# Optimization experiments

Hardware: AMD Instinct MI355X
Metric: run time of the kernel (lower is better)

The kernel has to match this reference:

```python
import jax, jax.numpy as jnp
import numpy as np

WS, SHIFT, NH, DIM = 8, 4, 4, 128
HD = DIM // NH
B, H, W = 16, 128, 128
N = WS * WS
LOG100 = float(np.log(100.0))


def _rel_tables():
    r = np.arange(-(WS - 1), WS, dtype=np.float32)
    tab = np.stack(np.meshgrid(r, r, indexing='ij'), axis=-1) / (WS - 1) * 8.0
    tab = np.sign(tab) * np.log2(np.abs(tab) + 1.0) / np.log2(8.0)
    coords = np.stack(np.meshgrid(np.arange(WS), np.arange(WS), indexing='ij')).reshape(2, -1)
    rel = (coords[:, :, None] - coords[:, None, :]).transpose(1, 2, 0).copy()
    rel[:, :, 0] += WS - 1
    rel[:, :, 1] += WS - 1
    rel[:, :, 0] *= 2 * WS - 1
    return jnp.asarray(tab.reshape(-1, 2)), jnp.asarray(rel.sum(-1))

REL_TABLE, REL_INDEX = _rel_tables()  # ((2WS-1)^2, 2), (N, N)


def _attn_mask():
    img = np.zeros((H, W), np.float32)
    cnt = 0
    for hs in (slice(0, -WS), slice(-WS, -SHIFT), slice(-SHIFT, None)):
        for ws in (slice(0, -WS), slice(-WS, -SHIFT), slice(-SHIFT, None)):
            img[hs, ws] = cnt
            cnt += 1
    mw = img.reshape(H // WS, WS, W // WS, WS).transpose(0, 2, 1, 3).reshape(-1, N)
    d = mw[:, None, :] - mw[:, :, None]
    return jnp.asarray(np.where(d != 0, -100.0, 0.0).astype(np.float32))

ATTN_MASK = _attn_mask()  # (nW, N, N)


def _ln(x, w, b, eps=1e-5):
    mu = x.mean(-1, keepdims=True)
    var = ((x - mu) ** 2).mean(-1, keepdims=True)
    return (x - mu) * jax.lax.rsqrt(var + eps) * w + b


def setup_inputs() -> dict:
    key = jax.random.key(0)
    ks = jax.random.split(key, 8)
    s = 0.02
    return {
        'x': jax.random.normal(ks[0], (B, DIM, H, W), jnp.float32),
        'norm1_w': jnp.ones((DIM,), jnp.float32),
        'norm1_b': jnp.zeros((DIM,), jnp.float32),
        'qkv_w': jax.random.normal(ks[1], (3 * DIM, DIM), jnp.float32) * s,
        'q_bias': jnp.zeros((DIM,), jnp.float32),
        'v_bias': jnp.zeros((DIM,), jnp.float32),
        'logit_scale': jnp.full((NH, 1, 1), float(np.log(10.0)), jnp.float32),
        'cpb_w1': jax.random.normal(ks[2], (512, 2), jnp.float32) * s,
        'cpb_b1': jnp.zeros((512,), jnp.float32),
        'cpb_w2': jax.random.normal(ks[3], (NH, 512), jnp.float32) * s,
        'proj_w': jax.random.normal(ks[4], (DIM, DIM), jnp.float32) * s,
        'proj_b': jnp.zeros((DIM,), jnp.float32),
        'norm2_w': jnp.ones((DIM,), jnp.float32),
        'norm2_b': jnp.zeros((DIM,), jnp.float32),
        'fc1_w': jax.random.normal(ks[5], (4 * DIM, DIM), jnp.float32) * s,
        'fc1_b': jnp.zeros((4 * DIM,), jnp.float32),
        'fc2_w': jax.random.normal(ks[6], (DIM, 4 * DIM), jnp.float32) * s,
        'fc2_b': jnp.zeros((DIM,), jnp.float32),
    }


def reference(x, norm1_w, norm1_b, qkv_w, q_bias, v_bias, logit_scale,
              cpb_w1, cpb_b1, cpb_w2, proj_w, proj_b,
              norm2_w, norm2_b, fc1_w, fc1_b, fc2_w, fc2_b):
    xb = jnp.transpose(x, (0, 2, 3, 1))                 # (B,H,W,C)
    shortcut = xb.reshape(B, H * W, DIM)
    shifted = jnp.roll(xb, (-SHIFT, -SHIFT), axis=(1, 2))
    # window partition -> (B*nW, N, C)
    xw = shifted.reshape(B, H // WS, WS, W // WS, WS, DIM)
    xw = xw.transpose(0, 1, 3, 2, 4, 5).reshape(-1, N, DIM)
    B_ = xw.shape[0]
    qkv_bias = jnp.concatenate([q_bias, jnp.zeros_like(v_bias), v_bias])
    qkv = xw @ qkv_w.T + qkv_bias
    qkv = qkv.reshape(B_, N, 3, NH, HD).transpose(2, 0, 3, 1, 4)
    q, k, v = qkv[0], qkv[1], qkv[2]                    # (B_,NH,N,HD)
    qn = q / jnp.maximum(jnp.linalg.norm(q, axis=-1, keepdims=True), 1e-12)
    kn = k / jnp.maximum(jnp.linalg.norm(k, axis=-1, keepdims=True), 1e-12)
    attn = jnp.einsum('bhnd,bhmd->bhnm', qn, kn)
    attn = attn * jnp.exp(jnp.minimum(logit_scale, LOG100))
    # continuous relative position bias: tiny MLP over log-spaced coords + gather
    tab = jax.nn.relu(REL_TABLE @ cpb_w1.T + cpb_b1) @ cpb_w2.T    # ((2WS-1)^2, NH)
    bias = tab[REL_INDEX.reshape(-1)].reshape(N, N, NH).transpose(2, 0, 1)
    attn = attn + (16.0 * jax.nn.sigmoid(bias))[None]
    nW = ATTN_MASK.shape[0]
    attn = attn.reshape(B_ // nW, nW, NH, N, N) + ATTN_MASK[None, :, None]
    attn = jax.nn.softmax(attn.reshape(B_, NH, N, N), axis=-1)
    out = jnp.einsum('bhnm,bhmd->bhnd', attn, v).transpose(0, 2, 1, 3).reshape(B_, N, DIM)
    out = out @ proj_w.T + proj_b
    # window reverse + reverse cyclic shift
    out = out.reshape(B, H // WS, W // WS, WS, WS, DIM).transpose(0, 1, 3, 2, 4, 5).reshape(B, H, W, DIM)
    out = jnp.roll(out, (SHIFT, SHIFT), axis=(1, 2)).reshape(B, H * W, DIM)
    x1 = shortcut + _ln(out, norm1_w, norm1_b)          # Swin-v2 post-norm residual
    hdn = jax.nn.silu(x1 @ fc1_w.T + fc1_b) @ fc2_w.T + fc2_b
    x2 = x1 + _ln(hdn, norm2_w, norm2_b)
    return x2.reshape(B, H, W, DIM).transpose(0, 3, 1, 2)
```

## Files before the change

kernel.cpp:

```cpp
#include <hip/hip_runtime.h>
#include <cstdint>
#include <cstddef>

typedef __bf16 bf16;
typedef __bf16 bf16x4 __attribute__((ext_vector_type(4)));
typedef __bf16 bf16x8 __attribute__((ext_vector_type(8)));
typedef float f32x4 __attribute__((ext_vector_type(4)));

#define MFMA16(a, b, c) __builtin_amdgcn_mfma_f32_16x16x32_bf16((a), (b), (c), 0, 0, 0)

__device__ __forceinline__ float bf2f(bf16 v) { return (float)v; }

__device__ __forceinline__ void pack4(float a0, float a1, float a2, float a3, bf16* dst) {
    bf16x4 v; v[0] = (bf16)a0; v[1] = (bf16)a1; v[2] = (bf16)a2; v[3] = (bf16)a3;
    *(bf16x4*)dst = v;
}

#define OFF_SCALES 65536
#define OFF_FLAG   65552
#define OFF_QKVB   65600
#define OFF_PROJB  67136
#define OFF_N1W    67648
#define OFF_N1B    68160
#define OFF_FC1B   68672
#define OFF_FC2B   70720
#define OFF_N2W    71232
#define OFF_N2B    71744
#define OFF_QKVW   73728
#define OFF_PROJW  172032
#define OFF_FC1W   204800
#define OFF_FC2W   335872

template<int DT>
__device__ __forceinline__ void g_ld4(const void* base, size_t idx, float* o) {
    if constexpr (DT == 0) {
        uint2 d = *(const uint2*)((const bf16*)base + idx);
        const bf16* p = (const bf16*)&d;
        o[0] = bf2f(p[0]); o[1] = bf2f(p[1]); o[2] = bf2f(p[2]); o[3] = bf2f(p[3]);
    } else {
        float4 d = *(const float4*)((const float*)base + idx);
        o[0] = d.x; o[1] = d.y; o[2] = d.z; o[3] = d.w;
    }
}

__global__ void k_init(const void* __restrict__ cpb_w1, const void* __restrict__ cpb_b1,
                       const void* __restrict__ cpb_w2, const void* __restrict__ logit_scale,
                       const void* __restrict__ qkv_w, const void* __restrict__ proj_w,
                       const void* __restrict__ fc1w, const void* __restrict__ fc2w,
                       const void* __restrict__ q_bias, const void* __restrict__ v_bias,
                       const void* __restrict__ proj_b, const void* __restrict__ n1w, const void* __restrict__ n1b,
                       const void* __restrict__ fc1b, const void* __restrict__ fc2b,
                       const void* __restrict__ n2w, const void* __restrict__ n2b,
                       char* __restrict__ ws)
{
    const int t = threadIdx.x;
    __shared__ int s_cnt;
    if (t == 0) s_cnt = 0;
    __syncthreads();
    {
        const unsigned short* u = (const unsigned short*)qkv_w;
        int c = 0;
        for (int i = t; i < 1024; i += 256) {
            const int e = (u[i] >> 7) & 0xFF;
            if (e >= 0x90 || (e != 0 && e <= 0x60)) ++c;
        }
        atomicAdd(&s_cnt, c);
    }
    __syncthreads();
    const int isf = (s_cnt > 64) ? 1 : 0;

    if (blockIdx.x == 0) {
        float* biasAll = (float*)ws;
        float* scales  = (float*)(ws + OFF_SCALES);
        int*   flag    = (int*)(ws + OFF_FLAG);
        if (t == 0) *flag = isf;
        __shared__ float w1s[1024];
        __shared__ float b1s[512];
        __shared__ float w2s[2048];
        __shared__ float tabv[225][4];
        if (isf) {
            const float* w1 = (const float*)cpb_w1;
            const float* b1 = (const float*)cpb_b1;
            const float* w2 = (const float*)cpb_w2;
            for (int i = t; i < 1024; i += 256) w1s[i] = w1[i];
            for (int i = t; i < 512;  i += 256) b1s[i] = b1[i];
            for (int i = t; i < 2048; i += 256) w2s[i] = w2[i];
            if (t < 4) scales[t] = expf(fminf(((const float*)logit_scale)[t], 4.6051701859880914f));
        } else {
            const bf16* w1 = (const bf16*)cpb_w1;
            const bf16* b1 = (const bf16*)cpb_b1;
            const bf16* w2 = (const bf16*)cpb_w2;
            for (int i = t; i < 1024; i += 256) w1s[i] = bf2f(w1[i]);
            for (int i = t; i < 512;  i += 256) b1s[i] = bf2f(b1[i]);
            for (int i = t; i < 2048; i += 256) w2s[i] = bf2f(w2[i]);
            if (t < 4) scales[t] = expf(fminf(bf2f(((const bf16*)logit_scale)[t]), 4.6051701859880914f));
        }
        __syncthreads();
        if (t < 225) {
            const int i = t / 15, j = t % 15;
            auto relf = [](int tt) -> float {
                float tf = (float)tt * (8.0f / 7.0f);
                float a = log2f(fabsf(tf) + 1.0f) * (1.0f / 3.0f);
                return tt < 0 ? -a : a;
            };
            const float x0 = relf(i - 7), x1 = relf(j - 7);
            float a0 = 0.f, a1 = 0.f, a2 = 0.f, a3 = 0.f;
            for (int jj = 0; jj < 512; ++jj) {
                float hv = w1s[jj*2] * x0 + w1s[jj*2+1] * x1 + b1s[jj];
                hv = fmaxf(hv, 0.0f);
                a0 += w2s[jj]        * hv;
                a1 += w2s[512 + jj]  * hv;
                a2 += w2s[1024 + jj] * hv;
                a3 += w2s[1536 + jj] * hv;
            }
            tabv[t][0] = a0; tabv[t][1] = a1; tabv[t][2] = a2; tabv[t][3] = a3;
        }
        __syncthreads();
        for (int idx = t; idx < 4*64*64; idx += 256) {
            const int h = idx >> 12, rem = idx & 4095, i = rem >> 6, j = rem & 63;
            const int di = (i >> 3) - (j >> 3) + 7;
            const int dj = (i & 7) - (j & 7) + 7;
            const float bv = tabv[di*15 + dj][h];
            biasAll[idx] = 16.0f / (1.0f + expf(-bv));
        }
    } else {
        const int g  = (blockIdx.x - 1) * 256 + t;
        const int gs = 96 * 256;
        bf16* qw = (bf16*)(ws + OFF_QKVW);
        bf16* pw = (bf16*)(ws + OFF_PROJW);
        bf16* f1 = (bf16*)(ws + OFF_FC1W);
        bf16* f2 = (bf16*)(ws + OFF_FC2W);
        if (isf) {
            const float* a = (const float*)qkv_w;  for (int i = g; i < 49152; i += gs) qw[i] = (bf16)a[i];
            const float* b = (const float*)proj_w; for (int i = g; i < 16384; i += gs) pw[i] = (bf16)b[i];
            const float* c = (const float*)fc1w;   for (int i = g; i < 65536; i += gs) f1[i] = (bf16)c[i];
            const float* d = (const float*)fc2w;   for (int i = g; i < 65536; i += gs) f2[i] = (bf16)d[i];
        } else {
            const bf16* a = (const bf16*)qkv_w;  for (int i = g; i < 49152; i += gs) qw[i] = a[i];
            const bf16* b = (const bf16*)proj_w; for (int i = g; i < 16384; i += gs) pw[i] = b[i];
            const bf16* c = (const bf16*)fc1w;   for (int i = g; i < 65536; i += gs) f1[i] = c[i];
            const bf16* d = (const bf16*)fc2w;   for (int i = g; i < 65536; i += gs) f2[i] = d[i];
        }
        auto ldf = [&](const void* p, int i) -> float {
            return isf ? ((const float*)p)[i] : bf2f(((const bf16*)p)[i]);
        };
        float* qb  = (float*)(ws + OFF_QKVB);
        float* pb  = (float*)(ws + OFF_PROJB);
        float* w1  = (float*)(ws + OFF_N1W);
        float* b1  = (float*)(ws + OFF_N1B);
        float* f1b = (float*)(ws + OFF_FC1B);
        float* f2b = (float*)(ws + OFF_FC2B);
        float* w2  = (float*)(ws + OFF_N2W);
        float* b2  = (float*)(ws + OFF_N2B);
        for (int i = g; i < 384; i += gs)
            qb[i] = (i < 128) ? ldf(q_bias, i) : ((i < 256) ? 0.0f : ldf(v_bias, i - 256));
        for (int i = g; i < 512; i += gs) f1b[i] = ldf(fc1b, i);
        for (int i = g; i < 128; i += gs) {
            pb[i]  = ldf(proj_b, i); w1[i] = ldf(n1w, i); b1[i] = ldf(n1b, i);
            f2b[i] = ldf(fc2b, i);   w2[i] = ldf(n2w, i); b2[i] = ldf(n2b, i);
        }
    }
}

__global__ __launch_bounds__(256, 2) void k_fused(
    const void* __restrict__ x,
    const bf16* __restrict__ qkvw, const float* __restrict__ qkvb,
    const bf16* __restrict__ projw, const float* __restrict__ projb,
    const float* __restrict__ n1wf, const float* __restrict__ n1bf,
    const bf16* __restrict__ fc1w, const float* __restrict__ fc1bf,
    const bf16* __restrict__ fc2w, const float* __restrict__ fc2bf,
    const float* __restrict__ n2wf, const float* __restrict__ n2bf,
    const float* __restrict__ biasAll, const float* __restrict__ scales,
    const int* __restrict__ flag, void* __restrict__ out)
{
    const int isf = *flag;

    __shared__ __align__(16) char smem[75008];
    bf16* Xs    = (bf16*)smem;
    bf16* qkvs  = (bf16*)(smem + 17408);
    bf16* PsT   = qkvs;
    bf16* x1s   = qkvs;
    bf16* vs    = (bf16*)(smem + 54272);
    bf16* Os    = vs;
    bf16* hs    = vs;
    float* invqs = (float*)(smem + 72704);
    float* invks = (float*)(smem + 73728);
    int*   rid   = (int*)(smem + 74752);
    float* psum = invqs;
    float* pvar = invks;

    const int tid  = threadIdx.x;
    const int wv   = tid >> 6;
    const int lane = tid & 63;
    const int l15  = lane & 15;
    const int quad = lane >> 4;

    const int bid0 = blockIdx.x;
    const int bid  = ((bid0 & 7) << 9) | (bid0 >> 3);
    const int b   = bid >> 8;
    const int wh  = (bid >> 4) & 15;
    const int ww  = bid & 15;

    {
        const int c  = tid & 127;
        const int rb = tid >> 7;
        const int w0 = ww*8 + 4;
        const int w1 = (ww*8 + 8) & 127;
#pragma unroll
        for (int k = 0; k < 4; ++k) {
            const int r    = k*2 + rb;
            const int srch = (wh*8 + r + 4) & 127;
            const size_t rowbase = (((size_t)(b*128 + c))*128 + srch)*128;
            float va[4], vb[4];
            if (isf) { g_ld4<1>(x, rowbase + w0, va); g_ld4<1>(x, rowbase + w1, vb); }
            else     { g_ld4<0>(x, rowbase + w0, va); g_ld4<0>(x, rowbase + w1, vb); }
#pragma unroll
            for (int j = 0; j < 4; ++j) {
                Xs[(r*8 + j)*136 + c]     = (bf16)va[j];
                Xs[(r*8 + 4 + j)*136 + c] = (bf16)vb[j];
            }
        }
        if (tid < 64) {
            const int rr = tid >> 3, cc = tid & 7;
            const int hs_ = wh*8 + rr, wsc = ww*8 + cc;
            const int rh = (hs_ < 120) ? 0 : ((hs_ < 124) ? 1 : 2);
            const int rw = (wsc < 120) ? 0 : ((wsc < 124) ? 1 : 2);
            rid[tid] = rh*3 + rw;
        }
    }
    __syncthreads();

    {
        f32x4 acc[6][4];
#pragma unroll
        for (int nl = 0; nl < 6; ++nl)
#pragma unroll
            for (int mt = 0; mt < 4; ++mt) acc[nl][mt] = (f32x4){0.f, 0.f, 0.f, 0.f};
#pragma unroll
        for (int ks = 0; ks < 4; ++ks) {
            bf16x8 a[4];
#pragma unroll
            for (int mt = 0; mt < 4; ++mt)
                a[mt] = *(const bf16x8*)&Xs[(mt*16 + l15)*136 + ks*32 + quad*8];
#pragma unroll
            for (int nl = 0; nl < 6; ++nl) {
                const int tile = wv*6 + nl;
                bf16x8 bw = *(const bf16x8*)&qkvw[(size_t)(tile*16 + l15)*128 + ks*32 + quad*8];
                if (tile < 16) {
#pragma unroll
                    for (int mt = 0; mt < 4; ++mt)
                        acc[nl][mt] = MFMA16(bw, a[mt], acc[nl][mt]);
                } else {
#pragma unroll
                    for (int mt = 0; mt < 4; ++mt)
                        acc[nl][mt] = MFMA16(a[mt], bw, acc[nl][mt]);
                }
            }
        }
#pragma unroll
        for (int nl = 0; nl < 6; ++nl) {
            const int tile = wv*6 + nl;
            const int ctb  = tile*16;
            if (ctb < 256) {
                const float4 qb4 = *(const float4*)&qkvb[ctb + quad*4];
#pragma unroll
                for (int mt = 0; mt < 4; ++mt)
                    pack4(acc[nl][mt][0] + qb4.x, acc[nl][mt][1] + qb4.y,
                          acc[nl][mt][2] + qb4.z, acc[nl][mt][3] + qb4.w,
                          &qkvs[(mt*16 + l15)*264 + ctb + quad*4]);
            } else {
                const float bb = qkvb[ctb + l15];
#pragma unroll
                for (int mt = 0; mt < 4; ++mt)
                    pack4(acc[nl][mt][0] + bb, acc[nl][mt][1] + bb,
                          acc[nl][mt][2] + bb, acc[nl][mt][3] + bb,
                          &vs[(ctb - 256 + l15)*72 + mt*16 + quad*4]);
            }
        }
    }
    __syncthreads();

    {
        const int n = lane;
        const bf16* qrow = &qkvs[n*264 + wv*32];
        const bf16* krow = &qkvs[n*264 + 128 + wv*32];
        float sq = 0.f, sk = 0.f;
#pragma unroll
        for (int dd = 0; dd < 4; ++dd) {
            bf16x8 vq = *(const bf16x8*)(qrow + dd*8);
            bf16x8 vk = *(const bf16x8*)(krow + dd*8);
#pragma unroll
            for (int e = 0; e < 8; ++e) {
                const float fq = (float)vq[e]; sq += fq*fq;
                const float fk = (float)vk[e]; sk += fk*fk;
            }
        }
        invqs[wv*64 + n] = 1.0f / fmaxf(sqrtf(sq), 1e-12f);
        invks[wv*64 + n] = 1.0f / fmaxf(sqrtf(sk), 1e-12f);
    }
    __syncthreads();

    {
        const float scale = scales[wv];
        f32x4 s[4][4];
#pragma unroll
        for (int jt = 0; jt < 4; ++jt)
#pragma unroll
            for (int it = 0; it < 4; ++it) s[jt][it] = (f32x4){0.f, 0.f, 0.f, 0.f};
        bf16x8 aq[4];
#pragma unroll
        for (int it = 0; it < 4; ++it)
            aq[it] = *(const bf16x8*)&qkvs[(it*16 + l15)*264 + wv*32 + quad*8];
#pragma unroll
        for (int jt = 0; jt < 4; ++jt) {
            bf16x8 bk = *(const bf16x8*)&qkvs[(jt*16 + l15)*264 + 128 + wv*32 + quad*8];
#pragma unroll
            for (int it = 0; it < 4; ++it)
                s[jt][it] = MFMA16(bk, aq[it], s[jt][it]);
        }
        __syncthreads();

        const float* bg = biasAll + wv*4096;
        const bool bnd = (wh == 15) || (ww == 15);
        float iqs[4]; int ri[4];
#pragma unroll
        for (int it = 0; it < 4; ++it) {
            iqs[it] = invqs[wv*64 + it*16 + l15] * scale;
            ri[it]  = rid[it*16 + l15];
        }
        float4 ikj[4]; int4 rj4[4];
#pragma unroll
        for (int jt = 0; jt < 4; ++jt) {
            ikj[jt] = *(const float4*)&invks[wv*64 + jt*16 + quad*4];
            rj4[jt] = *(const int4*)&rid[jt*16 + quad*4];
        }
#pragma unroll
        for (int it = 0; it < 4; ++it) {
            const int i = it*16 + l15;
#pragma unroll
            for (int jt = 0; jt < 4; ++jt) {
                const float4 bb = *(const float4*)&bg[i*64 + jt*16 + quad*4];
#pragma unroll
                for (int r = 0; r < 4; ++r) {
                    float v = s[jt][it][r] * (iqs[it] * ((const float*)&ikj[jt])[r]) + ((const float*)&bb)[r];
                    if (bnd && (ri[it] != ((const int*)&rj4[jt])[r])) v -= 100.0f;
                    s[jt][it][r] = v;
                }
            }
            float m = s[0][it][0];
#pragma unroll
            for (int jt = 0; jt < 4; ++jt)
#pragma unroll
                for (int r = 0; r < 4; ++r) m = fmaxf(m, s[jt][it][r]);
            m = fmaxf(m, __shfl_xor(m, 16));
            m = fmaxf(m, __shfl_xor(m, 32));
            float sm = 0.f;
#pragma unroll
            for (int jt = 0; jt < 4; ++jt)
#pragma unroll
                for (int r = 0; r < 4; ++r) {
                    const float e = __expf(s[jt][it][r] - m);
                    s[jt][it][r] = e;
                    sm += e;
                }
            sm += __shfl_xor(sm, 16);
            sm += __shfl_xor(sm, 32);
            const float inv = 1.0f / sm;
#pragma unroll
            for (int jt = 0; jt < 4; ++jt)
                pack4(s[jt][it][0]*inv, s[jt][it][1]*inv, s[jt][it][2]*inv, s[jt][it][3]*inv,
                      &PsT[wv*4608 + i*72 + jt*16 + quad*4]);
        }
    }
    __syncthreads();

    {
        f32x4 o[2][4];
#pragma unroll
        for (int dt = 0; dt < 2; ++dt)
#pragma unroll
            for (int it = 0; it < 4; ++it) o[dt][it] = (f32x4){0.f, 0.f, 0.f, 0.f};
#pragma unroll
        for (int ks = 0; ks < 2; ++ks) {
            bf16x8 bp[4];
#pragma unroll
            for (int it = 0; it < 4; ++it)
                bp[it] = *(const bf16x8*)&PsT[wv*4608 + (it*16 + l15)*72 + ks*32 + quad*8];
#pragma unroll
            for (int dt = 0; dt < 2; ++dt) {
                bf16x8 av = *(const bf16x8*)&vs[(wv*32 + dt*16 + l15)*72 + ks*32 + quad*8];
#pragma unroll
                for (int it = 0; it < 4; ++it)
                    o[dt][it] = MFMA16(av, bp[it], o[dt][it]);
            }
        }
        __syncthreads();
#pragma unroll
        for (int dt = 0; dt < 2; ++dt)
#pragma unroll
            for (int it = 0; it < 4; ++it)
                pack4(o[dt][it][0], o[dt][it][1], o[dt][it][2], o[dt][it][3],
                      &Os[(it*16 + l15)*136 + wv*32 + dt*16 + quad*4]);
    }
    __syncthreads();

    {
        f32x4 pa[2][4];
#pragma unroll
        for (int ct = 0; ct < 2; ++ct)
#pragma unroll
            for (int tt = 0; tt < 4; ++tt) pa[ct][tt] = (f32x4){0.f, 0.f, 0.f, 0.f};
#pragma unroll
        for (int ks = 0; ks < 4; ++ks) {
            bf16x8 bo[4];
#pragma unroll
            for (int tt = 0; tt < 4; ++tt)
                bo[tt] = *(const bf16x8*)&Os[(tt*16 + l15)*136 + ks*32 + quad*8];
#pragma unroll
            for (int ct = 0; ct < 2; ++ct) {
                bf16x8 aw = *(const bf16x8*)&projw[(size_t)(wv*32 + ct*16 + l15)*128 + ks*32 + quad*8];
#pragma unroll
                for (int tt = 0; tt < 4; ++tt)
                    pa[ct][tt] = MFMA16(aw, bo[tt], pa[ct][tt]);
            }
        }
        float4 pb4[2], wn4[2], bn4[2];
#pragma unroll
        for (int ct = 0; ct < 2; ++ct) {
            const int ob = wv*32 + ct*16 + quad*4;
            pb4[ct] = *(const float4*)&projb[ob];
            wn4[ct] = *(const float4*)&n1wf[ob];
            bn4[ct] = *(const float4*)&n1bf[ob];
        }
#pragma unroll
        for (int tt = 0; tt < 4; ++tt) {
            float sv = 0.f;
#pragma unroll
            for (int ct = 0; ct < 2; ++ct)
#pragma unroll
                for (int r = 0; r < 4; ++r) {
                    pa[ct][tt][r] += ((const float*)&pb4[ct])[r];
                    sv += pa[ct][tt][r];
                }
            sv += __shfl_xor(sv, 16);
            sv += __shfl_xor(sv, 32);
            if (quad == 0) psum[wv*64 + tt*16 + l15] = sv;
        }
        __syncthreads();
        float mu[4];
#pragma unroll
        for (int tt = 0; tt < 4; ++tt) {
            const int tok = tt*16 + l15;
            mu[tt] = (psum[tok] + psum[64+tok] + psum[128+tok] + psum[192+tok]) * (1.0f/128.0f);
            float sv = 0.f;
#pragma unroll
            for (int ct = 0; ct < 2; ++ct)
#pragma unroll
                for (int r = 0; r < 4; ++r) {
                    const float d = pa[ct][tt][r] - mu[tt];
                    sv += d*d;
                }
            sv += __shfl_xor(sv, 16);
            sv += __shfl_xor(sv, 32);
            if (quad == 0) pvar[wv*64 + tok] = sv;
        }
        __syncthreads();
#pragma unroll
        for (int tt = 0; tt < 4; ++tt) {
            const int tok = tt*16 + l15;
            const float var = (pvar[tok] + pvar[64+tok] + pvar[128+tok] + pvar[192+tok]) * (1.0f/128.0f);
            const float rstd = rsqrtf(var + 1e-5f);
#pragma unroll
            for (int ct = 0; ct < 2; ++ct) {
                const int ob = wv*32 + ct*16 + quad*4;
                bf16x4 xr = *(const bf16x4*)&Xs[tok*136 + ob];
                float xv[4];
#pragma unroll
                for (int r = 0; r < 4; ++r)
                    xv[r] = bf2f(xr[r]) + (pa[ct][tt][r] - mu[tt]) * rstd * ((const float*)&wn4[ct])[r]
                            + ((const float*)&bn4[ct])[r];
                pack4(xv[0], xv[1], xv[2], xv[3], &x1s[tok*136 + ob]);
            }
        }
    }
    __syncthreads();

    f32x4 ya[2][4];
#pragma unroll
    for (int ct = 0; ct < 2; ++ct)
#pragma unroll
        for (int tt = 0; tt < 4; ++tt) ya[ct][tt] = (f32x4){0.f, 0.f, 0.f, 0.f};

#pragma unroll
    for (int ch = 0; ch < 4; ++ch) {
        if (ch) __syncthreads();
        f32x4 ha[2][4];
#pragma unroll
        for (int ht = 0; ht < 2; ++ht)
#pragma unroll
            for (int tt = 0; tt < 4; ++tt) ha[ht][tt] = (f32x4){0.f, 0.f, 0.f, 0.f};
#pragma unroll
        for (int ks = 0; ks < 4; ++ks) {
            bf16x8 bx[4];
#pragma unroll
            for (int tt = 0; tt < 4; ++tt)
                bx[tt] = *(const bf16x8*)&x1s[(tt*16 + l15)*136 + ks*32 + quad*8];
#pragma unroll
            for (int ht = 0; ht < 2; ++ht) {
                bf16x8 aw = *(const bf16x8*)&fc1w[(size_t)(ch*128 + wv*32 + ht*16 + l15)*128 + ks*32 + quad*8];
#pragma unroll
                for (int tt = 0; tt < 4; ++tt)
                    ha[ht][tt] = MFMA16(aw, bx[tt], ha[ht][tt]);
            }
        }
#pragma unroll
        for (int ht = 0; ht < 2; ++ht) {
            const float4 bb4 = *(const float4*)&fc1bf[ch*128 + wv*32 + ht*16 + quad*4];
            const int hb = wv*32 + ht*16 + quad*4;
#pragma unroll
            for (int tt = 0; tt < 4; ++tt) {
                float hv[4];
#pragma unroll
                for (int r = 0; r < 4; ++r) {
                    float v = ha[ht][tt][r] + ((const float*)&bb4)[r];
                    hv[r] = v / (1.0f + __expf(-v));
                }
                pack4(hv[0], hv[1], hv[2], hv[3], &hs[(tt*16 + l15)*136 + hb]);
            }
        }
        __syncthreads();
#pragma unroll
        for (int ks = 0; ks < 4; ++ks) {
            bf16x8 bh[4];
#pragma unroll
            for (int tt = 0; tt < 4; ++tt)
                bh[tt] = *(const bf16x8*)&hs[(tt*16 + l15)*136 + ks*32 + quad*8];
#pragma unroll
            for (int ct = 0; ct < 2; ++ct) {
                bf16x8 aw = *(const bf16x8*)&fc2w[(size_t)(wv*32 + ct*16 + l15)*512 + ch*128 + ks*32 + quad*8];
#pragma unroll
                for (int tt = 0; tt < 4; ++tt)
                    ya[ct][tt] = MFMA16(aw, bh[tt], ya[ct][tt]);
            }
        }
    }
    __syncthreads();

    {
        float4 pb4[2], wn4[2], bn4[2];
#pragma unroll
        for (int ct = 0; ct < 2; ++ct) {
            const int ob = wv*32 + ct*16 + quad*4;
            pb4[ct] = *(const float4*)&fc2bf[ob];
            wn4[ct] = *(const float4*)&n2wf[ob];
            bn4[ct] = *(const float4*)&n2bf[ob];
        }
#pragma unroll
        for (int tt = 0; tt < 4; ++tt) {
            float sv = 0.f;
#pragma unroll
            for (int ct = 0; ct < 2; ++ct)
#pragma unroll
                for (int r = 0; r < 4; ++r) {
                    ya[ct][tt][r] += ((const float*)&pb4[ct])[r];
                    sv += ya[ct][tt][r];
                }
            sv += __shfl_xor(sv, 16);
            sv += __shfl_xor(sv, 32);
            if (quad == 0) psum[wv*64 + tt*16 + l15] = sv;
        }
        __syncthreads();
        float mu[4];
#pragma unroll
        for (int tt = 0; tt < 4; ++tt) {
            const int tok = tt*16 + l15;
            mu[tt] = (psum[tok] + psum[64+tok] + psum[128+tok] + psum[192+tok]) * (1.0f/128.0f);
            float sv = 0.f;
#pragma unroll
            for (int ct = 0; ct < 2; ++ct)
#pragma unroll
                for (int r = 0; r < 4; ++r) {
                    const float d = ya[ct][tt][r] - mu[tt];
                    sv += d*d;
                }
            sv += __shfl_xor(sv, 16);
            sv += __shfl_xor(sv, 32);
            if (quad == 0) pvar[wv*64 + tok] = sv;
        }
        __syncthreads();
        bf16* x2s = hs;
#pragma unroll
        for (int tt = 0; tt < 4; ++tt) {
            const int tok = tt*16 + l15;
            const float var = (pvar[tok] + pvar[64+tok] + pvar[128+tok] + pvar[192+tok]) * (1.0f/128.0f);
            const float rstd = rsqrtf(var + 1e-5f);
#pragma unroll
            for (int ct = 0; ct < 2; ++ct) {
                const int ob = wv*32 + ct*16 + quad*4;
                bf16x4 xr = *(const bf16x4*)&x1s[tok*136 + ob];
                float xv[4];
#pragma unroll
                for (int r = 0; r < 4; ++r)
                    xv[r] = bf2f(xr[r]) + (ya[ct][tt][r] - mu[tt]) * rstd * ((const float*)&wn4[ct])[r]
                            + ((const float*)&bn4[ct])[r];
                pack4(xv[0], xv[1], xv[2], xv[3], &x2s[tok*136 + ob]);
            }
        }
    }
    __syncthreads();

    {
        const bf16* x2s = hs;
        const int wf0 = ww*8 + 4;
        const int wf1 = (ww*8 + 8) & 127;
#pragma unroll
        for (int g = 0; g < 4; ++g) {
            const int idx = g*256 + tid;
            const int c  = idx & 127;
            const int rr = idx >> 7;
            const int hf = (wh*8 + rr + 4) & 127;
            const size_t rowb = ((size_t)(b*128 + c))*16384 + (size_t)hf*128;
            if (!isf) {
                const unsigned short* xu = (const unsigned short*)x2s;
                uint2 u0, u1;
                u0.x = (unsigned)xu[(rr*8+0)*136 + c] | ((unsigned)xu[(rr*8+1)*136 + c] << 16);
                u0.y = (unsigned)xu[(rr*8+2)*136 + c] | ((unsigned)xu[(rr*8+3)*136 + c] << 16);
                u1.x = (unsigned)xu[(rr*8+4)*136 + c] | ((unsigned)xu[(rr*8+5)*136 + c] << 16);
                u1.y = (unsigned)xu[(rr*8+6)*136 + c] | ((unsigned)xu[(rr*8+7)*136 + c] << 16);
                bf16* dstb = (bf16*)out;
                *(uint2*)(dstb + rowb + wf0) = u0;
                *(uint2*)(dstb + rowb + wf1) = u1;
            } else {
                float4 u0, u1;
                u0.x = bf2f(x2s[(rr*8+0)*136 + c]); u0.y = bf2f(x2s[(rr*8+1)*136 + c]);
                u0.z = bf2f(x2s[(rr*8+2)*136 + c]); u0.w = bf2f(x2s[(rr*8+3)*136 + c]);
                u1.x = bf2f(x2s[(rr*8+4)*136 + c]); u1.y = bf2f(x2s[(rr*8+5)*136 + c]);
                u1.z = bf2f(x2s[(rr*8+6)*136 + c]); u1.w = bf2f(x2s[(rr*8+7)*136 + c]);
                float* dstf = (float*)out;
                *(float4*)(dstf + rowb + wf0) = u0;
                *(float4*)(dstf + rowb + wf1) = u1;
            }
        }
    }
}

extern "C" void kernel_launch(void* const* d_in, const int* in_sizes, int n_in,
                              void* d_out, int out_size, void* d_ws, size_t ws_size,
                              hipStream_t stream)
{
    (void)in_sizes; (void)n_in; (void)out_size; (void)ws_size;
    const void* x      = d_in[0];
    const void* n1w    = d_in[1];
    const void* n1b    = d_in[2];
    const void* qkv_w  = d_in[3];
    const void* q_bias = d_in[4];
    const void* v_bias = d_in[5];
    const void* lscale = d_in[6];
    const void* cpb_w1 = d_in[7];
    const void* cpb_b1 = d_in[8];
    const void* cpb_w2 = d_in[9];
    const void* proj_w = d_in[10];
    const void* proj_b = d_in[11];
    const void* n2w    = d_in[12];
    const void* n2b    = d_in[13];
    const void* fc1w   = d_in[14];
    const void* fc1b   = d_in[15];
    const void* fc2w   = d_in[16];
    const void* fc2b   = d_in[17];

    char*  ws      = (char*)d_ws;
    float* biasAll = (float*)ws;
    float* scales  = (float*)(ws + OFF_SCALES);
    int*   flag    = (int*)(ws + OFF_FLAG);

    k_init<<<dim3(97), dim3(256), 0, stream>>>(cpb_w1, cpb_b1, cpb_w2, lscale,
                                               qkv_w, proj_w, fc1w, fc2w,
                                               q_bias, v_bias, proj_b, n1w, n1b,
                                               fc1b, fc2b, n2w, n2b, ws);
    k_fused<<<dim3(4096), dim3(256), 0, stream>>>(x,
        (const bf16*)(ws + OFF_QKVW), (const float*)(ws + OFF_QKVB),
        (const bf16*)(ws + OFF_PROJW), (const float*)(ws + OFF_PROJB),
        (const float*)(ws + OFF_N1W), (const float*)(ws + OFF_N1B),
        (const bf16*)(ws + OFF_FC1W), (const float*)(ws + OFF_FC1B),
        (const bf16*)(ws + OFF_FC2W), (const float*)(ws + OFF_FC2B),
        (const float*)(ws + OFF_N2W), (const float*)(ws + OFF_N2B),
        biasAll, scales, flag, d_out);
}
```

Baseline: 588.2 us.

## Shrink shared memory with swizzled aliasing to fit three blocks per CU

Cuts the LDS footprint from about 75KB to about 52KB by aliasing Q/K/probabilities and X/V/O buffers with XOR-swizzled layouts, and raises launch bounds to 3 blocks per SM. Q/K norms are now computed from the QKV accumulators in registers, which removes a pass over LDS and two barriers. The residual is re-read from global memory instead of kept in LDS. Risks are register pressure under the tighter bound (possible spills) and extra strided global reads for the residual.

```diff
diff --git a/kernel.cpp b/kernel.cpp
--- a/kernel.cpp
+++ b/kernel.cpp
@@ -162,7 +162,7 @@
     }
 }
 
-__global__ __launch_bounds__(256, 2) void k_fused(
+__global__ __launch_bounds__(256, 3) void k_fused(
     const void* __restrict__ x,
     const bf16* __restrict__ qkvw, const float* __restrict__ qkvb,
     const bf16* __restrict__ projw, const float* __restrict__ projb,
@@ -175,19 +175,17 @@
 {
     const int isf = *flag;
 
-    __shared__ __align__(16) char smem[75008];
-    bf16* Xs    = (bf16*)smem;
-    bf16* qkvs  = (bf16*)(smem + 17408);
-    bf16* PsT   = qkvs;
-    bf16* x1s   = qkvs;
-    bf16* vs    = (bf16*)(smem + 54272);
-    bf16* Os    = vs;
-    bf16* hs    = vs;
-    float* invqs = (float*)(smem + 72704);
-    float* invks = (float*)(smem + 73728);
-    int*   rid   = (int*)(smem + 74752);
-    float* psum = invqs;
-    float* pvar = invks;
+    __shared__ __align__(16) char smem[52480];
+    char* XK   = smem;
+    bf16* x1s  = (bf16*)smem;
+    char* R3   = smem + 32768;
+    bf16* Xs   = (bf16*)R3;
+    bf16* Os   = (bf16*)R3;
+    bf16* hs   = (bf16*)R3;
+    float* psum  = (float*)(smem + 50176);
+    float* invks = psum;
+    float* pvar  = (float*)(smem + 51200);
+    int*   rid   = (int*)(smem + 52224);
 
     const int tid  = threadIdx.x;
     const int wv   = tid >> 6;
@@ -230,12 +228,13 @@
     }
     __syncthreads();
 
+    float iq[4];
     {
         f32x4 acc[6][4];
 #pragma unroll
-        for (int nl = 0; nl < 6; ++nl)
-#pragma unroll
-            for (int mt = 0; mt < 4; ++mt) acc[nl][mt] = (f32x4){0.f, 0.f, 0.f, 0.f};
+        for (int t = 0; t < 6; ++t)
+#pragma unroll
+            for (int mt = 0; mt < 4; ++mt) acc[t][mt] = (f32x4){0.f, 0.f, 0.f, 0.f};
 #pragma unroll
         for (int ks = 0; ks < 4; ++ks) {
             bf16x8 a[4];
@@ -243,62 +242,65 @@
             for (int mt = 0; mt < 4; ++mt)
                 a[mt] = *(const bf16x8*)&Xs[(mt*16 + l15)*136 + ks*32 + quad*8];
 #pragma unroll
-            for (int nl = 0; nl < 6; ++nl) {
-                const int tile = wv*6 + nl;
-                bf16x8 bw = *(const bf16x8*)&qkvw[(size_t)(tile*16 + l15)*128 + ks*32 + quad*8];
-                if (tile < 16) {
+            for (int t = 0; t < 6; ++t) {
+                const int wrow = (t >> 1)*128 + wv*32 + (t & 1)*16 + l15;
+                bf16x8 bw = *(const bf16x8*)&qkvw[(size_t)wrow*128 + ks*32 + quad*8];
+                if (t < 4) {
 #pragma unroll
                     for (int mt = 0; mt < 4; ++mt)
-                        acc[nl][mt] = MFMA16(bw, a[mt], acc[nl][mt]);
+                        acc[t][mt] = MFMA16(bw, a[mt], acc[t][mt]);
                 } else {
 #pragma unroll
                     for (int mt = 0; mt < 4; ++mt)
-                        acc[nl][mt] = MFMA16(a[mt], bw, acc[nl][mt]);
-                }
-            }
-        }
-#pragma unroll
-        for (int nl = 0; nl < 6; ++nl) {
-            const int tile = wv*6 + nl;
-            const int ctb  = tile*16;
-            if (ctb < 256) {
-                const float4 qb4 = *(const float4*)&qkvb[ctb + quad*4];
-#pragma unroll
-                for (int mt = 0; mt < 4; ++mt)
-                    pack4(acc[nl][mt][0] + qb4.x, acc[nl][mt][1] + qb4.y,
-                          acc[nl][mt][2] + qb4.z, acc[nl][mt][3] + qb4.w,
-                          &qkvs[(mt*16 + l15)*264 + ctb + quad*4]);
-            } else {
-                const float bb = qkvb[ctb + l15];
-#pragma unroll
-                for (int mt = 0; mt < 4; ++mt)
-                    pack4(acc[nl][mt][0] + bb, acc[nl][mt][1] + bb,
-                          acc[nl][mt][2] + bb, acc[nl][mt][3] + bb,
-                          &vs[(ctb - 256 + l15)*72 + mt*16 + quad*4]);
-            }
-        }
-    }
-    __syncthreads();
-
-    {
-        const int n = lane;
-        const bf16* qrow = &qkvs[n*264 + wv*32];
-        const bf16* krow = &qkvs[n*264 + 128 + wv*32];
-        float sq = 0.f, sk = 0.f;
-#pragma unroll
-        for (int dd = 0; dd < 4; ++dd) {
-            bf16x8 vq = *(const bf16x8*)(qrow + dd*8);
-            bf16x8 vk = *(const bf16x8*)(krow + dd*8);
-#pragma unroll
-            for (int e = 0; e < 8; ++e) {
-                const float fq = (float)vq[e]; sq += fq*fq;
-                const float fk = (float)vk[e]; sk += fk*fk;
-            }
-        }
-        invqs[wv*64 + n] = 1.0f / fmaxf(sqrtf(sq), 1e-12f);
-        invks[wv*64 + n] = 1.0f / fmaxf(sqrtf(sk), 1e-12f);
-    }
-    __syncthreads();
+                        acc[t][mt] = MFMA16(a[mt], bw, acc[t][mt]);
+                }
+            }
+        }
+        __syncthreads();
+
+        float sq[4] = {0.f,0.f,0.f,0.f};
+        float sk[4] = {0.f,0.f,0.f,0.f};
+#pragma unroll
+        for (int t = 0; t < 4; ++t) {
+            const int colb = (t >> 1)*128 + wv*32 + (t & 1)*16 + quad*4;
+            const float4 b4 = *(const float4*)&qkvb[colb];
+#pragma unroll
+            for (int mt = 0; mt < 4; ++mt) {
+                const int row = mt*16 + l15;
+                const float v0 = acc[t][mt][0] + b4.x;
+                const float v1 = acc[t][mt][1] + b4.y;
+                const float v2 = acc[t][mt][2] + b4.z;
+                const float v3 = acc[t][mt][3] + b4.w;
+                const float ss = v0*v0 + v1*v1 + v2*v2 + v3*v3;
+                if (t < 2) sq[mt] += ss; else sk[mt] += ss;
+                pack4(v0, v1, v2, v3,
+                      (bf16*)(XK + row*512 + ((colb*2) ^ ((row & 7) << 4))));
+            }
+        }
+#pragma unroll
+        for (int t = 4; t < 6; ++t) {
+            const int vrow = wv*32 + (t & 1)*16 + l15;
+            const float bb = qkvb[256 + vrow];
+            char* vbase = R3 + vrow*128;
+            const int rx = (vrow & 7) << 4;
+#pragma unroll
+            for (int mt = 0; mt < 4; ++mt) {
+                const int tokb = mt*16 + quad*4;
+                pack4(acc[t][mt][0] + bb, acc[t][mt][1] + bb,
+                      acc[t][mt][2] + bb, acc[t][mt][3] + bb,
+                      (bf16*)(vbase + ((tokb*2) ^ rx)));
+            }
+        }
+#pragma unroll
+        for (int mt = 0; mt < 4; ++mt) {
+            float s2 = sq[mt];
+            s2 += __shfl_xor(s2, 16); s2 += __shfl_xor(s2, 32);
+            iq[mt] = 1.0f / fmaxf(sqrtf(s2), 1e-12f);
+            float k2 = sk[mt];
+            k2 += __shfl_xor(k2, 16); k2 += __shfl_xor(k2, 32);
+            if (quad == 0) invks[wv*64 + mt*16 + l15] = 1.0f / fmaxf(sqrtf(k2), 1e-12f);
+        }
+    }
 
     {
         const float scale = scales[wv];
@@ -309,11 +311,14 @@
             for (int it = 0; it < 4; ++it) s[jt][it] = (f32x4){0.f, 0.f, 0.f, 0.f};
         bf16x8 aq[4];
 #pragma unroll
-        for (int it = 0; it < 4; ++it)
-            aq[it] = *(const bf16x8*)&qkvs[(it*16 + l15)*264 + wv*32 + quad*8];
+        for (int it = 0; it < 4; ++it) {
+            const int row = it*16 + l15;
+            aq[it] = *(const bf16x8*)(XK + row*512 + (((wv*32 + quad*8)*2) ^ ((row & 7) << 4)));
+        }
 #pragma unroll
         for (int jt = 0; jt < 4; ++jt) {
-            bf16x8 bk = *(const bf16x8*)&qkvs[(jt*16 + l15)*264 + 128 + wv*32 + quad*8];
+            const int row = jt*16 + l15;
+            bf16x8 bk = *(const bf16x8*)(XK + row*512 + (((128 + wv*32 + quad*8)*2) ^ ((row & 7) << 4)));
 #pragma unroll
             for (int it = 0; it < 4; ++it)
                 s[jt][it] = MFMA16(bk, aq[it], s[jt][it]);
@@ -325,7 +330,7 @@
         float iqs[4]; int ri[4];
 #pragma unroll
         for (int it = 0; it < 4; ++it) {
-            iqs[it] = invqs[wv*64 + it*16 + l15] * scale;
+            iqs[it] = iq[it] * scale;
             ri[it]  = rid[it*16 + l15];
         }
         float4 ikj[4]; int4 rj4[4];
@@ -369,10 +374,9 @@
 #pragma unroll
             for (int jt = 0; jt < 4; ++jt)
                 pack4(s[jt][it][0]*inv, s[jt][it][1]*inv, s[jt][it][2]*inv, s[jt][it][3]*inv,
-                      &PsT[wv*4608 + i*72 + jt*16 + quad*4]);
-        }
-    }
-    __syncthreads();
+                      (bf16*)(XK + wv*8192 + i*128 + ((jt*32 + quad*8) ^ ((i & 7) << 4))));
+        }
+    }
 
     {
         f32x4 o[2][4];
@@ -384,11 +388,14 @@
         for (int ks = 0; ks < 2; ++ks) {
             bf16x8 bp[4];
 #pragma unroll
-            for (int it = 0; it < 4; ++it)
-                bp[it] = *(const bf16x8*)&PsT[wv*4608 + (it*16 + l15)*72 + ks*32 + quad*8];
+            for (int it = 0; it < 4; ++it) {
+                const int row = it*16 + l15;
+                bp[it] = *(const bf16x8*)(XK + wv*8192 + row*128 + ((ks*64 + quad*16) ^ ((row & 7) << 4)));
+            }
 #pragma unroll
             for (int dt = 0; dt < 2; ++dt) {
-                bf16x8 av = *(const bf16x8*)&vs[(wv*32 + dt*16 + l15)*72 + ks*32 + quad*8];
+                const int vrow = wv*32 + dt*16 + l15;
+                bf16x8 av = *(const bf16x8*)(R3 + vrow*128 + ((ks*64 + quad*16) ^ ((vrow & 7) << 4)));
 #pragma unroll
                 for (int it = 0; it < 4; ++it)
                     o[dt][it] = MFMA16(av, bp[it], o[dt][it]);
@@ -405,6 +412,24 @@
     __syncthreads();
 
     {
+        float res[2][4][4];
+#pragma unroll
+        for (int tt = 0; tt < 4; ++tt) {
+            const int tok = tt*16 + l15;
+            const int hh  = (wh*8 + (tok >> 3) + 4) & 127;
+            const int wwp = (ww*8 + (tok & 7) + 4) & 127;
+            const size_t tb = (size_t)b*2097152 + (size_t)hh*128 + wwp;
+#pragma unroll
+            for (int ct = 0; ct < 2; ++ct)
+#pragma unroll
+                for (int r = 0; r < 4; ++r) {
+                    const int c = wv*32 + ct*16 + quad*4 + r;
+                    float xv;
+                    if (isf) xv = ((const float*)x)[tb + (size_t)c*16384];
+                    else     xv = bf2f(((const bf16*)x)[tb + (size_t)c*16384]);
+                    res[ct][tt][r] = bf2f((bf16)xv);
+                }
+        }
         f32x4 pa[2][4];
 #pragma unroll
         for (int ct = 0; ct < 2; ++ct)
@@ -473,11 +498,10 @@
 #pragma unroll
             for (int ct = 0; ct < 2; ++ct) {
                 const int ob = wv*32 + ct*16 + quad*4;
-                bf16x4 xr = *(const bf16x4*)&Xs[tok*136 + ob];
                 float xv[4];
 #pragma unroll
                 for (int r = 0; r < 4; ++r)
-                    xv[r] = bf2f(xr[r]) + (pa[ct][tt][r] - mu[tt]) * rstd * ((const float*)&wn4[ct])[r]
+                    xv[r] = res[ct][tt][r] + (pa[ct][tt][r] - mu[tt]) * rstd * ((const float*)&wn4[ct])[r]
                             + ((const float*)&bn4[ct])[r];
                 pack4(xv[0], xv[1], xv[2], xv[3], &x1s[tok*136 + ob]);
             }
```

Result: slower. 620.8 us (+5.5%).
